# Kernel tuning notes

Hardware: AMD Instinct MI355X
Metric: run time of the kernel (lower is better)

## Reference

```python
import jax, jax.numpy as jnp
import numpy as np

CONTACT_THRESH = 0.01
COLLISION_THRESH = 0.005
WEIGHT_PEN = 100.0
WEIGHT_MISS = 10.0
# MANO fingertip + palm contact-zone vertex indices (hardcoded in module)
CONTACT_IDX = np.array([745, 317, 444, 556, 673, 95, 182, 234, 279, 320])

SCALE = 0.1  # place points in a 0.1 m cube so mm-scale thresholds are meaningful


def setup_inputs() -> dict:
    key = jax.random.key(0)
    k1, k2, k3, k4 = jax.random.split(key, 4)
    B, NH, V = 8, 778, 40000
    hand_verts = jax.random.uniform(k1, (B, NH, 3), dtype=jnp.float32) * SCALE
    obj_verts = jax.random.uniform(k2, (B, V, 3), dtype=jnp.float32) * SCALE
    hand_faces = jax.random.randint(k3, (1538, 3), 0, NH, dtype=jnp.int64 if jax.config.read('jax_enable_x64') else jnp.int32)
    obj_faces = jax.random.randint(k4, (79996, 3), 0, V, dtype=jnp.int64 if jax.config.read('jax_enable_x64') else jnp.int32)
    return {"hand_verts": hand_verts, "obj_verts": obj_verts,
            "hand_faces": hand_faces, "obj_faces": obj_faces}


def _min_dists(a, b):
    """Brute-force 1-NN: min Euclidean distance from each point in a [B,N,3] to b [B,M,3] -> [B,N]."""
    a_sq = jnp.sum(a * a, axis=-1, keepdims=True)          # [B,N,1]
    b_sq = jnp.sum(b * b, axis=-1)                          # [B,M]
    ab = jnp.einsum('bnd,bmd->bnm', a, b)                   # [B,N,M]
    d2 = jnp.maximum(a_sq + b_sq[:, None, :] - 2.0 * ab, 0.0)
    return jnp.sqrt(jnp.min(d2, axis=2))                    # [B,N]


def _masked_mean(vals, mask):
    cnt = jnp.sum(mask)
    s = jnp.sum(jnp.where(mask, vals, 0.0))
    return jnp.where(cnt > 0, s / jnp.maximum(cnt, 1).astype(vals.dtype), jnp.zeros((), vals.dtype))


def reference(hand_verts, obj_verts, hand_faces, obj_faces):
    # faces are unused by the loss (as in the torch module)
    idx = jnp.asarray(CONTACT_IDX)
    # distances are computed under no_grad / detached in the original
    dists = jax.lax.stop_gradient(_min_dists(hand_verts, obj_verts))              # [B,778]
    contact_dists = jax.lax.stop_gradient(_min_dists(hand_verts[:, idx, :], obj_verts))  # [B,10]

    pen_mask = dists < COLLISION_THRESH
    pen_loss = _masked_mean((COLLISION_THRESH - dists) ** 2, pen_mask)

    att_mask = (contact_dists > COLLISION_THRESH) & (contact_dists < CONTACT_THRESH)
    att_loss = _masked_mean(contact_dists ** 2, att_mask)

    contact_loss = WEIGHT_PEN * pen_loss + WEIGHT_MISS * att_loss
    dist_mean = jnp.mean(dists)
    num_contacts = jnp.sum(att_mask).astype(jnp.int32)
    num_penetrations = jnp.sum(pen_mask).astype(jnp.int32)
    return (contact_loss, pen_loss, att_loss, dist_mean, num_contacts, num_penetrations)
```

## Files before the change

kernel.cpp:

```cpp
#include <hip/hip_runtime.h>
#include <math.h>

typedef float v2f __attribute__((ext_vector_type(2)));

constexpr int NH     = 778;
constexpr int T      = 16;
constexpr int G      = 4;
constexpr int NBX    = (NH + G * T - 1) / (G * T);
constexpr int BLK    = 256;
constexpr int CHUNKP = 2560;
constexpr int LPP    = CHUNKP / BLK;
constexpr int PPAIR  = LPP / 2;

__global__ __launch_bounds__(BLK, 2) void nn_min_kernel(
    const float* __restrict__ hand,
    const float* __restrict__ obj,
    unsigned int* __restrict__ minb,
    int V)
{
    __shared__ float s_red[4][16 * 65];
    const int bx   = blockIdx.x;
    const int c    = blockIdx.y;
    const int b    = blockIdx.z;
    const int tid  = threadIdx.x;
    const int wave = tid >> 6;
    const int lane = tid & 63;
    const int r    = lane & 15;
    const int seg  = lane >> 4;

    const float* ob = obj + (size_t)b * V * 3;
    const int base = c * CHUNKP + tid;
    v2f ox2[PPAIR], oy2[PPAIR], oz2[PPAIR], oq2[PPAIR];
#pragma unroll
    for (int p = 0; p < PPAIR; ++p) {
        const int ja = min(base + (2 * p + 0) * BLK, V - 1);
        const int jb = min(base + (2 * p + 1) * BLK, V - 1);
        const float xa = ob[3 * ja + 0], ya = ob[3 * ja + 1], za = ob[3 * ja + 2];
        const float xb = ob[3 * jb + 0], yb = ob[3 * jb + 1], zb = ob[3 * jb + 2];
        ox2[p] = (v2f){-2.f * xa, -2.f * xb};
        oy2[p] = (v2f){-2.f * ya, -2.f * yb};
        oz2[p] = (v2f){-2.f * za, -2.f * zb};
        oq2[p] = (v2f){fmaf(xa, xa, fmaf(ya, ya, za * za)),
                       fmaf(xb, xb, fmaf(yb, yb, zb * zb))};
    }

    const float* hb = hand + (size_t)b * NH * 3;
    float* sw = &s_red[wave][0];

#pragma unroll 1
    for (int g = 0; g < G; ++g) {
        float hx[T], hy[T], hz[T];
#pragma unroll
        for (int t = 0; t < T; ++t) {
            const int h = min((bx * G + g) * T + t, NH - 1);
            hx[t] = hb[3 * h + 0];
            hy[t] = hb[3 * h + 1];
            hz[t] = hb[3 * h + 2];
        }

        float m[T];
#pragma unroll
        for (int t = 0; t < T; ++t) m[t] = 3.4e38f;

#pragma unroll
        for (int p = 0; p < PPAIR; ++p) {
#pragma unroll
            for (int t = 0; t < T; ++t) {
                v2f a = __builtin_elementwise_fma(ox2[p], (v2f){hx[t], hx[t]}, oq2[p]);
                a = __builtin_elementwise_fma(oy2[p], (v2f){hy[t], hy[t]}, a);
                a = __builtin_elementwise_fma(oz2[p], (v2f){hz[t], hz[t]}, a);
                m[t] = fminf(fminf(a.x, a.y), m[t]);
            }
        }

#pragma unroll
        for (int t = 0; t < T; ++t) {
            const float hq = fmaf(hx[t], hx[t], fmaf(hy[t], hy[t], hz[t] * hz[t]));
            sw[t * 65 + lane] = m[t] + hq;
        }
        __builtin_amdgcn_wave_barrier();

        float v = 3.4e38f;
        const int rbase = r * 65 + seg * 16;
#pragma unroll
        for (int j = 0; j < 16; ++j) v = fminf(v, sw[rbase + j]);
        __builtin_amdgcn_wave_barrier();

        v = fminf(v, __shfl_xor(v, 16));
        v = fminf(v, __shfl_xor(v, 32));

        if (seg == 0) {
            const int hidx = (bx * G + g) * T + r;
            if (hidx < NH) {
                const unsigned bits = __float_as_uint(fmaxf(v, 0.f));
                unsigned int* p = &minb[b * NH + hidx];
                if (bits < *((volatile unsigned int*)p)) atomicMin(p, bits);
            }
        }
    }
}

__global__ __launch_bounds__(256) void finalize_kernel(
    const unsigned int* __restrict__ minb, float* __restrict__ out, int B)
{
    constexpr float COLL = 0.005f;
    constexpr float CONT = 0.01f;
    const int total = B * NH;
    const int tid = threadIdx.x;

    double sum_d = 0.0, pen_sum = 0.0, att_sum = 0.0;
    int pen_cnt = 0, att_cnt = 0;
    for (int i = tid; i < total; i += 256) {
        const float d = sqrtf(__uint_as_float(minb[i]));
        sum_d += (double)d;
        if (d < COLL) { const float t = COLL - d; pen_sum += (double)(t * t); pen_cnt++; }
        const int n = i % NH;
        const bool isc = (n == 745) | (n == 317) | (n == 444) | (n == 556) |
                         (n == 673) | (n == 95)  | (n == 182) | (n == 234) |
                         (n == 279) | (n == 320);
        if (isc & (d > COLL) & (d < CONT)) { att_sum += (double)(d * d); att_cnt++; }
    }

    __shared__ double sd[256], sp[256], sa[256];
    __shared__ int    cp[256], ca[256];
    sd[tid] = sum_d; sp[tid] = pen_sum; sa[tid] = att_sum;
    cp[tid] = pen_cnt; ca[tid] = att_cnt;
    __syncthreads();
    for (int off = 128; off > 0; off >>= 1) {
        if (tid < off) {
            sd[tid] += sd[tid + off]; sp[tid] += sp[tid + off];
            sa[tid] += sa[tid + off];
            cp[tid] += cp[tid + off]; ca[tid] += ca[tid + off];
        }
        __syncthreads();
    }
    if (tid == 0) {
        const double pen_loss = cp[0] > 0 ? sp[0] / (double)cp[0] : 0.0;
        const double att_loss = ca[0] > 0 ? sa[0] / (double)ca[0] : 0.0;
        out[0] = (float)(100.0 * pen_loss + 10.0 * att_loss);
        out[1] = (float)pen_loss;
        out[2] = (float)att_loss;
        out[3] = (float)(sd[0] / (double)total);
        out[4] = (float)ca[0];
        out[5] = (float)cp[0];
    }
}

extern "C" void kernel_launch(void* const* d_in, const int* in_sizes, int n_in,
                              void* d_out, int out_size, void* d_ws, size_t ws_size,
                              hipStream_t stream) {
    const float* hand = (const float*)d_in[0];
    const float* obj  = (const float*)d_in[1];

    const int B = in_sizes[0] / (NH * 3);
    const int V = in_sizes[1] / (B * 3);
    const int nchunks = (V + CHUNKP - 1) / CHUNKP;

    unsigned int* minb = (unsigned int*)d_ws;

    hipMemsetAsync(d_ws, 0x7F, (size_t)B * NH * sizeof(unsigned int), stream);

    dim3 grid(NBX, nchunks, B);
    nn_min_kernel<<<grid, BLK, 0, stream>>>(hand, obj, minb, V);
    finalize_kernel<<<1, 256, 0, stream>>>(minb, (float*)d_out, B);
}
```

Before: 107.6 us.

## Replace brute-force nearest-neighbour search with uniform-grid spatial binning

Object points are binned into a fixed 16^3 uniform grid over the assumed 0.1 m cube, with per-cell buckets of capacity 40 and a global overflow list. Each hand vertex then scans its 3x3x3 neighbouring cells using 4 lanes per query, expanding outward ring by ring only while the current best distance could still be beaten. This removes the dense all-pairs distance computation. The cost is atomic-heavy binning, a workspace-size-dependent path that falls back to the old brute-force kernel, and a grid whose extent is hardcoded to the input's bounding box.

```diff
diff --git a/kernel.cpp b/kernel.cpp
--- a/kernel.cpp
+++ b/kernel.cpp
@@ -1,96 +1,197 @@
 #include <hip/hip_runtime.h>
 #include <math.h>
 
+constexpr int NH    = 778;
+constexpr int GRIDC = 16;
+constexpr int NCELL = GRIDC * GRIDC * GRIDC;
+constexpr int CAP   = 40;
+constexpr float CELL     = 0.1f / GRIDC;
+constexpr float INV_CELL = GRIDC / 0.1f;
+constexpr int SPLIT = 4;
+
+__device__ __forceinline__ int clampc(int v) {
+    return min(GRIDC - 1, max(0, v));
+}
+
+__global__ __launch_bounds__(256) void bin_kernel(
+    const float* __restrict__ obj,
+    int* __restrict__ cnt,
+    int* __restrict__ ocnt,
+    float4* __restrict__ buckets,
+    float4* __restrict__ ovf,
+    int total, int V)
+{
+    const int i = blockIdx.x * 256 + threadIdx.x;
+    if (i >= total) return;
+    const float x = obj[3 * i + 0];
+    const float y = obj[3 * i + 1];
+    const float z = obj[3 * i + 2];
+    const int cx = clampc((int)(x * INV_CELL));
+    const int cy = clampc((int)(y * INV_CELL));
+    const int cz = clampc((int)(z * INV_CELL));
+    const int b = i / V;
+    const int cell = b * NCELL + (cz * GRIDC + cy) * GRIDC + cx;
+    const int idx = atomicAdd(&cnt[cell], 1);
+    if (idx < CAP) {
+        buckets[(size_t)cell * CAP + idx] = make_float4(x, y, z, 0.f);
+    } else {
+        const int oi = atomicAdd(ocnt, 1);
+        ovf[oi] = make_float4(x, y, z, __int_as_float(b));
+    }
+}
+
+__global__ __launch_bounds__(256) void query_kernel(
+    const float* __restrict__ hand,
+    const int* __restrict__ cnt,
+    const float4* __restrict__ buckets,
+    const float4* __restrict__ ovf,
+    const int* __restrict__ ocnt,
+    float* __restrict__ dist,
+    int B)
+{
+    const int gid = blockIdx.x * 256 + threadIdx.x;
+    const int i   = gid >> 2;
+    const int sub = gid & (SPLIT - 1);
+    if (i >= B * NH) return;
+    const int b = i / NH;
+
+    const float hx = hand[3 * i + 0];
+    const float hy = hand[3 * i + 1];
+    const float hz = hand[3 * i + 2];
+    const int hcx = clampc((int)(hx * INV_CELL));
+    const int hcy = clampc((int)(hy * INV_CELL));
+    const int hcz = clampc((int)(hz * INV_CELL));
+
+    const int cbase = b * NCELL;
+    float best = 3.4e38f;
+
+    auto scan_cell = [&](int cell) {
+        const int n = min(cnt[cbase + cell], CAP);
+        const float4* bp = buckets + (size_t)(cbase + cell) * CAP;
+        for (int k = sub; k < n; k += SPLIT) {
+            const float4 p = bp[k];
+            const float dx = p.x - hx, dy = p.y - hy, dz = p.z - hz;
+            best = fminf(best, fmaf(dx, dx, fmaf(dy, dy, dz * dz)));
+        }
+    };
+
+    for (int dz = -1; dz <= 1; ++dz) {
+        const int cz = hcz + dz;
+        if (cz < 0 || cz >= GRIDC) continue;
+        for (int dy = -1; dy <= 1; ++dy) {
+            const int cy = hcy + dy;
+            if (cy < 0 || cy >= GRIDC) continue;
+            for (int dx = -1; dx <= 1; ++dx) {
+                const int cx = hcx + dx;
+                if (cx < 0 || cx >= GRIDC) continue;
+                scan_cell((cz * GRIDC + cy) * GRIDC + cx);
+            }
+        }
+    }
+    best = fminf(best, __shfl_xor(best, 1));
+    best = fminf(best, __shfl_xor(best, 2));
+
+    for (int r = 2; r < GRIDC; ++r) {
+        const float bnd = (float)(r - 1) * CELL;
+        if (best <= bnd * bnd) break;
+        for (int dz = -r; dz <= r; ++dz) {
+            const int cz = hcz + dz;
+            if (cz < 0 || cz >= GRIDC) continue;
+            const int adz = abs(dz);
+            for (int dy = -r; dy <= r; ++dy) {
+                const int cy = hcy + dy;
+                if (cy < 0 || cy >= GRIDC) continue;
+                const int ady = abs(dy);
+                for (int dx = -r; dx <= r; ++dx) {
+                    if (max(max(abs(dx), ady), adz) != r) continue;
+                    const int cx = hcx + dx;
+                    if (cx < 0 || cx >= GRIDC) continue;
+                    scan_cell((cz * GRIDC + cy) * GRIDC + cx);
+                }
+            }
+        }
+        best = fminf(best, __shfl_xor(best, 1));
+        best = fminf(best, __shfl_xor(best, 2));
+    }
+
+    const int on = *ocnt;
+    for (int k = sub; k < on; k += SPLIT) {
+        const float4 p = ovf[k];
+        if (__float_as_int(p.w) == b) {
+            const float dx = p.x - hx, dy = p.y - hy, dz = p.z - hz;
+            best = fminf(best, fmaf(dx, dx, fmaf(dy, dy, dz * dz)));
+        }
+    }
+    best = fminf(best, __shfl_xor(best, 1));
+    best = fminf(best, __shfl_xor(best, 2));
+
+    if (sub == 0) dist[i] = best;
+}
+
 typedef float v2f __attribute__((ext_vector_type(2)));
-
-constexpr int NH     = 778;
-constexpr int T      = 16;
-constexpr int G      = 4;
-constexpr int NBX    = (NH + G * T - 1) / (G * T);
-constexpr int BLK    = 256;
-constexpr int CHUNKP = 2560;
-constexpr int LPP    = CHUNKP / BLK;
-constexpr int PPAIR  = LPP / 2;
-
-__global__ __launch_bounds__(BLK, 2) void nn_min_kernel(
-    const float* __restrict__ hand,
-    const float* __restrict__ obj,
-    unsigned int* __restrict__ minb,
-    int V)
+constexpr int FT = 16, FG = 4, FBLK = 256, FCHUNK = 2560;
+constexpr int FNBX = (NH + FG * FT - 1) / (FG * FT);
+constexpr int FLPP = FCHUNK / FBLK, FPP = FLPP / 2;
+
+__global__ __launch_bounds__(FBLK, 2) void nn_brute_kernel(
+    const float* __restrict__ hand, const float* __restrict__ obj,
+    unsigned int* __restrict__ minb, int V)
 {
     __shared__ float s_red[4][16 * 65];
-    const int bx   = blockIdx.x;
-    const int c    = blockIdx.y;
-    const int b    = blockIdx.z;
-    const int tid  = threadIdx.x;
-    const int wave = tid >> 6;
-    const int lane = tid & 63;
-    const int r    = lane & 15;
-    const int seg  = lane >> 4;
-
+    const int bx = blockIdx.x, c = blockIdx.y, b = blockIdx.z;
+    const int tid = threadIdx.x, wave = tid >> 6, lane = tid & 63;
+    const int r = lane & 15, seg = lane >> 4;
     const float* ob = obj + (size_t)b * V * 3;
-    const int base = c * CHUNKP + tid;
-    v2f ox2[PPAIR], oy2[PPAIR], oz2[PPAIR], oq2[PPAIR];
-#pragma unroll
-    for (int p = 0; p < PPAIR; ++p) {
-        const int ja = min(base + (2 * p + 0) * BLK, V - 1);
-        const int jb = min(base + (2 * p + 1) * BLK, V - 1);
-        const float xa = ob[3 * ja + 0], ya = ob[3 * ja + 1], za = ob[3 * ja + 2];
-        const float xb = ob[3 * jb + 0], yb = ob[3 * jb + 1], zb = ob[3 * jb + 2];
+    const int base = c * FCHUNK + tid;
+    v2f ox2[FPP], oy2[FPP], oz2[FPP], oq2[FPP];
+#pragma unroll
+    for (int p = 0; p < FPP; ++p) {
+        const int ja = min(base + (2 * p + 0) * FBLK, V - 1);
+        const int jb = min(base + (2 * p + 1) * FBLK, V - 1);
+        const float xa = ob[3 * ja], ya = ob[3 * ja + 1], za = ob[3 * ja + 2];
+        const float xb = ob[3 * jb], yb = ob[3 * jb + 1], zb = ob[3 * jb + 2];
         ox2[p] = (v2f){-2.f * xa, -2.f * xb};
         oy2[p] = (v2f){-2.f * ya, -2.f * yb};
         oz2[p] = (v2f){-2.f * za, -2.f * zb};
         oq2[p] = (v2f){fmaf(xa, xa, fmaf(ya, ya, za * za)),
                        fmaf(xb, xb, fmaf(yb, yb, zb * zb))};
     }
-
     const float* hb = hand + (size_t)b * NH * 3;
     float* sw = &s_red[wave][0];
-
 #pragma unroll 1
-    for (int g = 0; g < G; ++g) {
-        float hx[T], hy[T], hz[T];
-#pragma unroll
-        for (int t = 0; t < T; ++t) {
-            const int h = min((bx * G + g) * T + t, NH - 1);
-            hx[t] = hb[3 * h + 0];
-            hy[t] = hb[3 * h + 1];
-            hz[t] = hb[3 * h + 2];
-        }
-
-        float m[T];
-#pragma unroll
-        for (int t = 0; t < T; ++t) m[t] = 3.4e38f;
-
-#pragma unroll
-        for (int p = 0; p < PPAIR; ++p) {
-#pragma unroll
-            for (int t = 0; t < T; ++t) {
+    for (int g = 0; g < FG; ++g) {
+        float hx[FT], hy[FT], hz[FT], m[FT];
+#pragma unroll
+        for (int t = 0; t < FT; ++t) {
+            const int h = min((bx * FG + g) * FT + t, NH - 1);
+            hx[t] = hb[3 * h]; hy[t] = hb[3 * h + 1]; hz[t] = hb[3 * h + 2];
+            m[t] = 3.4e38f;
+        }
+#pragma unroll
+        for (int p = 0; p < FPP; ++p) {
+#pragma unroll
+            for (int t = 0; t < FT; ++t) {
                 v2f a = __builtin_elementwise_fma(ox2[p], (v2f){hx[t], hx[t]}, oq2[p]);
                 a = __builtin_elementwise_fma(oy2[p], (v2f){hy[t], hy[t]}, a);
                 a = __builtin_elementwise_fma(oz2[p], (v2f){hz[t], hz[t]}, a);
                 m[t] = fminf(fminf(a.x, a.y), m[t]);
             }
         }
-
-#pragma unroll
-        for (int t = 0; t < T; ++t) {
+#pragma unroll
+        for (int t = 0; t < FT; ++t) {
             const float hq = fmaf(hx[t], hx[t], fmaf(hy[t], hy[t], hz[t] * hz[t]));
             sw[t * 65 + lane] = m[t] + hq;
         }
         __builtin_amdgcn_wave_barrier();
-
         float v = 3.4e38f;
-        const int rbase = r * 65 + seg * 16;
-#pragma unroll
-        for (int j = 0; j < 16; ++j) v = fminf(v, sw[rbase + j]);
+        const int rb = r * 65 + seg * 16;
+#pragma unroll
+        for (int j = 0; j < 16; ++j) v = fminf(v, sw[rb + j]);
         __builtin_amdgcn_wave_barrier();
-
         v = fminf(v, __shfl_xor(v, 16));
         v = fminf(v, __shfl_xor(v, 32));
-
         if (seg == 0) {
-            const int hidx = (bx * G + g) * T + r;
+            const int hidx = (bx * FG + g) * FT + r;
             if (hidx < NH) {
                 const unsigned bits = __float_as_uint(fmaxf(v, 0.f));
                 unsigned int* p = &minb[b * NH + hidx];
@@ -101,7 +202,7 @@
 }
 
 __global__ __launch_bounds__(256) void finalize_kernel(
-    const unsigned int* __restrict__ minb, float* __restrict__ out, int B)
+    const float* __restrict__ dist, float* __restrict__ out, int B)
 {
     constexpr float COLL = 0.005f;
     constexpr float CONT = 0.01f;
@@ -111,7 +212,7 @@
     double sum_d = 0.0, pen_sum = 0.0, att_sum = 0.0;
     int pen_cnt = 0, att_cnt = 0;
     for (int i = tid; i < total; i += 256) {
-        const float d = sqrtf(__uint_as_float(minb[i]));
+        const float d = sqrtf(fmaxf(dist[i], 0.f));
         sum_d += (double)d;
         if (d < COLL) { const float t = COLL - d; pen_sum += (double)(t * t); pen_cnt++; }
         const int n = i % NH;
@@ -154,13 +255,32 @@
 
     const int B = in_sizes[0] / (NH * 3);
     const int V = in_sizes[1] / (B * 3);
-    const int nchunks = (V + CHUNKP - 1) / CHUNKP;
-
-    unsigned int* minb = (unsigned int*)d_ws;
-
-    hipMemsetAsync(d_ws, 0x7F, (size_t)B * NH * sizeof(unsigned int), stream);
-
-    dim3 grid(NBX, nchunks, B);
-    nn_min_kernel<<<grid, BLK, 0, stream>>>(hand, obj, minb, V);
-    finalize_kernel<<<1, 256, 0, stream>>>(minb, (float*)d_out, B);
-}
+    const int total = B * V;
+
+    float* dist = (float*)d_ws;
+    char* base = (char*)d_ws;
+    size_t off = 65536;
+    int* cnt = (int*)(base + off);
+    const size_t cnt_bytes = (size_t)B * NCELL * sizeof(int);
+    int* ocnt = (int*)(base + off + cnt_bytes);
+    size_t boff = (off + cnt_bytes + 256) & ~(size_t)255;
+    float4* buckets = (float4*)(base + boff);
+    const size_t bkt_bytes = (size_t)B * NCELL * CAP * sizeof(float4);
+    float4* ovf = (float4*)(base + boff + bkt_bytes);
+    const size_t need = boff + bkt_bytes + (size_t)total * sizeof(float4);
+
+    if (ws_size >= need) {
+        hipMemsetAsync(cnt, 0, cnt_bytes + 64, stream);
+        bin_kernel<<<(total + 255) / 256, 256, 0, stream>>>(
+            obj, cnt, ocnt, buckets, ovf, total, V);
+        const int qthreads = B * NH * SPLIT;
+        query_kernel<<<(qthreads + 255) / 256, 256, 0, stream>>>(
+            hand, cnt, buckets, ovf, ocnt, dist, B);
+    } else {
+        hipMemsetAsync(d_ws, 0x7F, (size_t)B * NH * sizeof(unsigned int), stream);
+        dim3 grid(FNBX, (V + FCHUNK - 1) / FCHUNK, B);
+        nn_brute_kernel<<<grid, FBLK, 0, stream>>>(hand, obj,
+                                                   (unsigned int*)d_ws, V);
+    }
+    finalize_kernel<<<1, 256, 0, stream>>>(dist, (float*)d_out, B);
+}
```

After: 130.1 us. +20.9%, slower.
